# Kernel optimization log

Measured on AMD Instinct MI355X. Metric: run time of the kernel, lower is better.

## Reference

```python
import jax, jax.numpy as jnp
import numpy as np
import math

B, H, W, D = 4, 64, 64, 256
N, K, V = 8, 32, 32


def setup_inputs() -> dict:
    key = jax.random.key(0)
    ks = jax.random.split(key, 7)
    blob = jax.random.normal(ks[0], (B, H, W, D), dtype=jnp.float32)
    # 1x1 conv kernels == dense [D, out] matrices; glorot-ish scale
    s = 1.0 / math.sqrt(D)
    wq = jax.random.normal(ks[1], (D, N * K), dtype=jnp.float32) * s
    wk = jax.random.normal(ks[2], (D, N * K), dtype=jnp.float32) * s
    wv = jax.random.normal(ks[3], (D, N * V), dtype=jnp.float32) * s
    bq = jnp.zeros((N * K,), jnp.float32)
    bk = jnp.zeros((N * K,), jnp.float32)
    bv = jnp.zeros((N * V,), jnp.float32)
    return {"blob": blob, "wq": wq, "bq": bq, "wk": wk, "bk": bk, "wv": wv, "bv": bv}


def _maxpool2x2(x):
    # MaxPool2D with pool_size=strides=(2,2), VALID padding, NHWC
    return jax.lax.reduce_window(
        x, -jnp.inf, jax.lax.max,
        window_dimensions=(1, 2, 2, 1), window_strides=(1, 2, 2, 1), padding="VALID")


def reference(blob, wq, bq, wk, bk, wv, bv):
    H2, W2 = H // 2, W // 2
    # pooled query path
    q = _maxpool2x2(blob)                                   # [B,H2,W2,D]
    q = (q @ wq + bq).reshape(B, H2, W2, N, K)              # [B,H2,W2,N,K]
    q = q * (1.0 / math.sqrt(float(K)))
    # key/value paths (1x1 conv == per-pixel matmul); swish on value
    k = (blob @ wk + bk).reshape(B, H * W, N, K)            # [B,HW,N,K]
    v = jax.nn.swish(blob @ wv + bv).reshape(B, H * W, N, V)  # [B,HW,N,V]
    # cross-attention: contract K, outer product of pooled grid with full grid
    scores = jnp.einsum("bhwnk,bink->bhwin", q, k)          # [B,H2,W2,HW,N]
    attn = jax.nn.softmax(scores, axis=3)                   # softmax over HW
    out = jnp.einsum("bhwin,binv->bhwnv", attn, v)          # [B,H2,W2,N,V]
    return out.reshape(B, H2, W2, N * V)
```

## Files before the change

kernel.cpp:

```cpp
#include <hip/hip_runtime.h>


typedef _Float16 f16x8 __attribute__((ext_vector_type(8)));
typedef _Float16 f16x4 __attribute__((ext_vector_type(4)));
typedef float    f32x4 __attribute__((ext_vector_type(4)));

#define F16(x) static_cast<_Float16>(x)

#if __has_builtin(__builtin_amdgcn_exp2f)
#define EXP2(x) __builtin_amdgcn_exp2f(x)
#else
#define EXP2(x) exp2f(x)
#endif

__device__ __forceinline__ void gl_lds16(const void* g, void* l) {
    __builtin_amdgcn_global_load_lds(
        (const __attribute__((address_space(1))) unsigned int*)g,
        (__attribute__((address_space(3))) unsigned int*)l, 16, 0, 0);
}

__global__ __launch_bounds__(256) void prep_kernel(
    const float* __restrict__ wq, const float* __restrict__ wk,
    const float* __restrict__ wv, _Float16* __restrict__ wt) {
    __shared__ float t[32][33];
    const int blk = blockIdx.x;
    const int mat = blk >> 6;
    const int tile = blk & 63;
    const int d0 = (tile >> 3) * 32, o0 = (tile & 7) * 32;
    const float* w = (mat == 0) ? wq : (mat == 1 ? wk : wv);
    const int tx = threadIdx.x & 31, ty = threadIdx.x >> 5;
#pragma unroll
    for (int i = 0; i < 4; ++i)
        t[ty + i * 8][tx] = w[(d0 + ty + i * 8) * 256 + o0 + tx];
    __syncthreads();
#pragma unroll
    for (int i = 0; i < 4; ++i)
        wt[(mat << 16) + (o0 + ty + i * 8) * 256 + d0 + tx] = (_Float16)t[tx][ty + i * 8];
}

__global__ __launch_bounds__(256) void proj_kernel(
    const float* __restrict__ blob, const _Float16* __restrict__ wt,
    const float* __restrict__ bq, const float* __restrict__ bk, const float* __restrict__ bv,
    _Float16* __restrict__ qo, _Float16* __restrict__ ko, _Float16* __restrict__ vo) {
    const int lane = threadIdx.x & 63, wid = threadIdx.x >> 6;
    const int quad = lane >> 4, l16 = lane & 15;
    int jb = blockIdx.x;
    int job, rowblk;
    if (jb < 128)      { job = 0; rowblk = jb; }
    else if (jb < 640) { job = 1; rowblk = jb - 128; }
    else               { job = 2; rowblk = jb - 640; }
    const int rowbase = rowblk * 32;
    const int colbase = wid * 64;
    const _Float16* wmat = wt + ((size_t)job << 16);
    const float* bias = (job == 0) ? bq : (job == 1 ? bk : bv);

    f32x4 acc[2][4];
#pragma unroll
    for (int mc = 0; mc < 2; ++mc)
#pragma unroll
        for (int nt = 0; nt < 4; ++nt) acc[mc][nt] = (f32x4){0.f, 0.f, 0.f, 0.f};

    const float* a0[2];
#pragma unroll
    for (int mc = 0; mc < 2; ++mc) {
        const int m = rowbase + mc * 16 + l16;
        if (job == 0) {
            const int bb = m >> 10, y = (m >> 5) & 31, x = m & 31;
            a0[mc] = blob + (((bb * 64 + 2 * y) * 64) + 2 * x) * 256;
        } else {
            a0[mc] = blob + (size_t)m * 256;
        }
    }

#pragma unroll 2
    for (int kc = 0; kc < 8; ++kc) {
        f16x8 bf[4];
#pragma unroll
        for (int nt = 0; nt < 4; ++nt)
            bf[nt] = *(const f16x8*)(wmat + (colbase + nt * 16 + l16) * 256 + kc * 32 + quad * 8);
#pragma unroll
        for (int mc = 0; mc < 2; ++mc) {
            const float* ap = a0[mc] + kc * 32 + quad * 8;
            float va[8];
            if (job == 0) {
                float4 p0 = *(const float4*)(ap);
                float4 p1 = *(const float4*)(ap + 4);
                float4 q0 = *(const float4*)(ap + 256);
                float4 q1 = *(const float4*)(ap + 260);
                float4 r0 = *(const float4*)(ap + 16384);
                float4 r1 = *(const float4*)(ap + 16388);
                float4 s0 = *(const float4*)(ap + 16640);
                float4 s1 = *(const float4*)(ap + 16644);
                va[0] = fmaxf(fmaxf(p0.x, q0.x), fmaxf(r0.x, s0.x));
                va[1] = fmaxf(fmaxf(p0.y, q0.y), fmaxf(r0.y, s0.y));
                va[2] = fmaxf(fmaxf(p0.z, q0.z), fmaxf(r0.z, s0.z));
                va[3] = fmaxf(fmaxf(p0.w, q0.w), fmaxf(r0.w, s0.w));
                va[4] = fmaxf(fmaxf(p1.x, q1.x), fmaxf(r1.x, s1.x));
                va[5] = fmaxf(fmaxf(p1.y, q1.y), fmaxf(r1.y, s1.y));
                va[6] = fmaxf(fmaxf(p1.z, q1.z), fmaxf(r1.z, s1.z));
                va[7] = fmaxf(fmaxf(p1.w, q1.w), fmaxf(r1.w, s1.w));
            } else {
                float4 f0 = *(const float4*)(ap);
                float4 f1 = *(const float4*)(ap + 4);
                va[0] = f0.x; va[1] = f0.y; va[2] = f0.z; va[3] = f0.w;
                va[4] = f1.x; va[5] = f1.y; va[6] = f1.z; va[7] = f1.w;
            }
            auto c0 = __builtin_amdgcn_cvt_pkrtz(va[0], va[1]);
            auto c1 = __builtin_amdgcn_cvt_pkrtz(va[2], va[3]);
            auto c2 = __builtin_amdgcn_cvt_pkrtz(va[4], va[5]);
            auto c3 = __builtin_amdgcn_cvt_pkrtz(va[6], va[7]);
            f16x8 af = {F16(c0[0]), F16(c0[1]), F16(c1[0]), F16(c1[1]),
                        F16(c2[0]), F16(c2[1]), F16(c3[0]), F16(c3[1])};
#pragma unroll
            for (int nt = 0; nt < 4; ++nt)
                acc[mc][nt] = __builtin_amdgcn_mfma_f32_16x16x32_f16(af, bf[nt], acc[mc][nt], 0, 0, 0);
        }
    }

#pragma unroll
    for (int nt = 0; nt < 4; ++nt) {
        const int o = colbase + nt * 16 + l16;
        const float bs = bias[o];
        const int nh = o >> 5, kk = o & 31;
#pragma unroll
        for (int mc = 0; mc < 2; ++mc) {
            if (job == 0) {
#pragma unroll
                for (int r = 0; r < 4; ++r) {
                    const int grow = rowbase + mc * 16 + quad * 4 + r;
                    const float x = (acc[mc][nt][r] + bs) * 0.25503508f;
                    const int bb = grow >> 10, mm = grow & 1023;
                    qo[(((bb * 8 + nh) * 1024 + mm) << 5) + kk] = (_Float16)x;
                }
            } else if (job == 1) {
#pragma unroll
                for (int r = 0; r < 4; ++r) {
                    const int grow = rowbase + mc * 16 + quad * 4 + r;
                    const float x = acc[mc][nt][r] + bs;
                    const int bb = grow >> 12, ii = grow & 4095;
                    ko[(((bb * 8 + nh) * 4096 + ii) << 5) + kk] = (_Float16)x;
                }
            } else {
                const int grow0 = rowbase + mc * 16 + quad * 4;
                const int bb = grow0 >> 12, i0 = grow0 & 4095;
                f16x4 pv;
#pragma unroll
                for (int r = 0; r < 4; ++r) {
                    float x = acc[mc][nt][r] + bs;
                    const float sg = 1.0f / (1.0f + __expf(-x));
                    pv[r] = (_Float16)(x * sg);
                }
                *(f16x4*)(vo + (((size_t)(bb * 8 + nh) * 32 + kk) << 12) + i0) = pv;
            }
        }
    }
}

__global__ __launch_bounds__(512, 4) void attn_kernel(
    const _Float16* __restrict__ qb,
    const _Float16* __restrict__ kb,
    const _Float16* __restrict__ vt,
    float* __restrict__ out) {
    __shared__ __align__(16) char pool[49152];

    const int tid = threadIdx.x;
    const int lane = tid & 63, wid = tid >> 6;
    const int quad = lane >> 4, l16 = lane & 15;
    const int bn = blockIdx.x & 31, mt = blockIdx.x >> 5;
    const int b = bn >> 3, n = bn & 7;
    const int m0 = mt * 64;
    const int rg = wid & 3, kc = wid >> 2;

    const _Float16* gsrc[2];
    int ldsoff[2], adv[2];
#pragma unroll
    for (int jj = 0; jj < 2; ++jj) {
        const int j = wid + jj * 8;
        const int kcj = j >> 3, sub = j & 7;
        const int gl = (sub & 3) * 64 + lane;
        if (sub < 4) {
            const int k = gl >> 2, c = ((gl & 3) - (k >> 2)) & 3;
            gsrc[jj]   = kb + ((size_t)bn << 17) + (size_t)(kcj * 2048 + k) * 32 + c * 8;
            ldsoff[jj] = kcj * 24576 + gl * 16;
            adv[jj] = 2048;
        } else {
            const int v = gl >> 3, c = ((gl & 7) - v) & 7;
            gsrc[jj]   = vt + ((size_t)bn << 17) + (size_t)v * 4096 + kcj * 2048 + c * 8;
            ldsoff[jj] = kcj * 24576 + 4096 + gl * 16;
            adv[jj] = 64;
        }
    }

    const f16x8 qf = *(const f16x8*)(qb + (((size_t)(bn << 10) + m0 + rg * 16 + l16) << 5) + quad * 8);

    const int kread = kc * 24576 + l16 * 64 + ((quad + (l16 >> 2)) & 3) * 16;
    const int vread = kc * 24576 + 4096 + l16 * 128 + (quad & 1) * 8;
    const int r0 = (quad >> 1) + l16;

#pragma unroll
    for (int p = 0; p < 2; ++p)
#pragma unroll
        for (int jj = 0; jj < 2; ++jj) {
            gl_lds16(gsrc[jj], pool + ldsoff[jj] + p * 8192);
            gsrc[jj] += adv[jj];
        }
    asm volatile("s_waitcnt vmcnt(2)\n\ts_barrier" ::: "memory");

    f32x4 acc0 = (f32x4){0.f, 0.f, 0.f, 0.f};
    f32x4 acc1 = acc0;
    float ps0 = 0.f;

    for (int s = 0; s < 32; ++s) {
        if (s < 30) {
            const int nb = ((s + 2) % 3) * 8192;
#pragma unroll
            for (int jj = 0; jj < 2; ++jj) {
                gl_lds16(gsrc[jj], pool + ldsoff[jj] + nb);
                gsrc[jj] += adv[jj];
            }
        }
        const char* kbase = pool + kread + (s % 3) * 8192;
        const char* vbase = pool + vread + (s % 3) * 8192;
#pragma unroll
        for (int tloc = 0; tloc < 4; ++tloc) {
            const f16x8 kf = *(const f16x8*)(kbase + tloc * 1024);
            const int rot = ((2 * tloc + r0) & 7) * 16;
            const f16x4 va0 = *(const f16x4*)(vbase + rot);
            const f16x4 va1 = *(const f16x4*)(vbase + rot + 2048);

            f32x4 s0 = __builtin_amdgcn_mfma_f32_16x16x32_f16(kf, qf, (f32x4){0.f,0.f,0.f,0.f}, 0, 0, 0);
            const float p0 = EXP2(s0[0]), p1 = EXP2(s0[1]), p2 = EXP2(s0[2]), p3 = EXP2(s0[3]);
            ps0 += (p0 + p1) + (p2 + p3);
            auto e0 = __builtin_amdgcn_cvt_pkrtz(p0, p1);
            auto e1 = __builtin_amdgcn_cvt_pkrtz(p2, p3);
            const f16x4 pb = {F16(e0[0]), F16(e0[1]), F16(e1[0]), F16(e1[1])};
            acc0 = __builtin_amdgcn_mfma_f32_16x16x16f16(va0, pb, acc0, 0, 0, 0);
            acc1 = __builtin_amdgcn_mfma_f32_16x16x16f16(va1, pb, acc1, 0, 0, 0);
        }
        if (s < 30)       asm volatile("s_waitcnt vmcnt(2)\n\ts_barrier" ::: "memory");
        else if (s == 30) asm volatile("s_waitcnt vmcnt(0)\n\ts_barrier" ::: "memory");
        else              asm volatile("s_barrier" ::: "memory");
    }

    float* num = (float*)pool;
    float* den = (float*)(pool + 64 * 33 * 4);
    for (int i = tid; i < 64 * 33 + 64; i += 512) ((float*)pool)[i] = 0.f;
    __syncthreads();

    ps0 += __shfl_xor(ps0, 16); ps0 += __shfl_xor(ps0, 32);

    const int m = rg * 16 + l16;
#pragma unroll
    for (int r = 0; r < 4; ++r) {
        atomicAdd(&num[m * 33 + quad * 4 + r], acc0[r]);
        atomicAdd(&num[m * 33 + 16 + quad * 4 + r], acc1[r]);
    }
    if (quad == 0) atomicAdd(&den[m], ps0);
    __syncthreads();

    {
        const int mloc = tid >> 3, v4 = (tid & 7) * 4;
        const float inv = 1.0f / den[mloc];
        const float* nr = num + mloc * 33 + v4;
        float4 o = {nr[0] * inv, nr[1] * inv, nr[2] * inv, nr[3] * inv};
        *(float4*)(out + (((size_t)(b << 10) + m0 + mloc) << 8) + n * 32 + v4) = o;
    }
}

extern "C" void kernel_launch(void* const* d_in, const int* in_sizes, int n_in,
                              void* d_out, int out_size, void* d_ws, size_t ws_size,
                              hipStream_t stream) {
    const float* blob = (const float*)d_in[0];
    const float* wq = (const float*)d_in[1];
    const float* bq = (const float*)d_in[2];
    const float* wk = (const float*)d_in[3];
    const float* bk = (const float*)d_in[4];
    const float* wv = (const float*)d_in[5];
    const float* bv = (const float*)d_in[6];
    float* out = (float*)d_out;

    char* ws = (char*)d_ws;
    _Float16* wt = (_Float16*)(ws);
    _Float16* ko = (_Float16*)(ws + 393216);
    _Float16* vo = (_Float16*)(ws + 8781824);
    _Float16* qo = (_Float16*)(ws + 17170432);

    prep_kernel<<<192, 256, 0, stream>>>(wq, wk, wv, wt);
    proj_kernel<<<1152, 256, 0, stream>>>(blob, wt, bq, bk, bv, qo, ko, vo);
    attn_kernel<<<512, 512, 0, stream>>>(qo, ko, vo, out);
}
```

Baseline: 161.6 us.

## Stage A tile through LDS with double buffering and 64-row blocks in projection

The projection kernel now covers 64 rows per block instead of 32, halving the grid. Each thread loads one 8-element fp32 slice of the activation (max-pooled for the query job), converts it to fp16 and writes it into a swizzled, double-buffered LDS tile. All four waves then read it from LDS instead of each wave reloading the activations from global memory. Weight fragments and the next activation slice are prefetched one step ahead around a barrier. This cuts redundant global activation traffic and overlaps loads with MFMA work, at the cost of per-step barriers, more accumulator registers and fewer blocks for latency hiding.

```diff
diff --git a/kernel.cpp b/kernel.cpp
--- a/kernel.cpp
+++ b/kernel.cpp
@@ -42,79 +42,108 @@
     const float* __restrict__ blob, const _Float16* __restrict__ wt,
     const float* __restrict__ bq, const float* __restrict__ bk, const float* __restrict__ bv,
     _Float16* __restrict__ qo, _Float16* __restrict__ ko, _Float16* __restrict__ vo) {
-    const int lane = threadIdx.x & 63, wid = threadIdx.x >> 6;
+    __shared__ __align__(16) char atile[2][4096];
+
+    const int tid = threadIdx.x;
+    const int lane = tid & 63, wid = tid >> 6;
     const int quad = lane >> 4, l16 = lane & 15;
     int jb = blockIdx.x;
     int job, rowblk;
-    if (jb < 128)      { job = 0; rowblk = jb; }
-    else if (jb < 640) { job = 1; rowblk = jb - 128; }
-    else               { job = 2; rowblk = jb - 640; }
-    const int rowbase = rowblk * 32;
+    if (jb < 64)       { job = 0; rowblk = jb; }
+    else if (jb < 320) { job = 1; rowblk = jb - 64; }
+    else               { job = 2; rowblk = jb - 320; }
+    const int rowbase = rowblk * 64;
     const int colbase = wid * 64;
     const _Float16* wmat = wt + ((size_t)job << 16);
     const float* bias = (job == 0) ? bq : (job == 1 ? bk : bv);
 
-    f32x4 acc[2][4];
-#pragma unroll
-    for (int mc = 0; mc < 2; ++mc)
+    const int srow = tid >> 2, sc8 = tid & 3;
+    const int sslot = srow * 4 + ((sc8 + (srow >> 2)) & 3);
+    const float* aptr;
+    if (job == 0) {
+        const int grow = rowbase + srow;
+        const int bb = grow >> 10, y = (grow >> 5) & 31, x = grow & 31;
+        aptr = blob + (((bb * 64 + 2 * y) * 64) + 2 * x) * 256 + sc8 * 8;
+    } else {
+        aptr = blob + (size_t)(rowbase + srow) * 256 + sc8 * 8;
+    }
+
+    const _Float16* wptr[4];
+#pragma unroll
+    for (int nt = 0; nt < 4; ++nt)
+        wptr[nt] = wmat + (size_t)(colbase + nt * 16 + l16) * 256 + quad * 8;
+
+    const int aread = l16 * 64 + ((quad + (l16 >> 2)) & 3) * 16;
+
+    f32x4 acc[4][4];
+#pragma unroll
+    for (int mc = 0; mc < 4; ++mc)
 #pragma unroll
         for (int nt = 0; nt < 4; ++nt) acc[mc][nt] = (f32x4){0.f, 0.f, 0.f, 0.f};
 
-    const float* a0[2];
-#pragma unroll
-    for (int mc = 0; mc < 2; ++mc) {
-        const int m = rowbase + mc * 16 + l16;
+    f16x8 wf[2][4];
+    float4 ar[2][2];
+
+    auto A_LOAD = [&](int t, float4* dst) {
+        const float* p = aptr + t * 32;
         if (job == 0) {
-            const int bb = m >> 10, y = (m >> 5) & 31, x = m & 31;
-            a0[mc] = blob + (((bb * 64 + 2 * y) * 64) + 2 * x) * 256;
+            float4 a0 = *(const float4*)(p);
+            float4 a1 = *(const float4*)(p + 4);
+            float4 b0 = *(const float4*)(p + 256);
+            float4 b1 = *(const float4*)(p + 260);
+            float4 c0 = *(const float4*)(p + 16384);
+            float4 c1 = *(const float4*)(p + 16388);
+            float4 d0 = *(const float4*)(p + 16640);
+            float4 d1 = *(const float4*)(p + 16644);
+            dst[0].x = fmaxf(fmaxf(a0.x, b0.x), fmaxf(c0.x, d0.x));
+            dst[0].y = fmaxf(fmaxf(a0.y, b0.y), fmaxf(c0.y, d0.y));
+            dst[0].z = fmaxf(fmaxf(a0.z, b0.z), fmaxf(c0.z, d0.z));
+            dst[0].w = fmaxf(fmaxf(a0.w, b0.w), fmaxf(c0.w, d0.w));
+            dst[1].x = fmaxf(fmaxf(a1.x, b1.x), fmaxf(c1.x, d1.x));
+            dst[1].y = fmaxf(fmaxf(a1.y, b1.y), fmaxf(c1.y, d1.y));
+            dst[1].z = fmaxf(fmaxf(a1.z, b1.z), fmaxf(c1.z, d1.z));
+            dst[1].w = fmaxf(fmaxf(a1.w, b1.w), fmaxf(c1.w, d1.w));
         } else {
-            a0[mc] = blob + (size_t)m * 256;
-        }
-    }
-
-#pragma unroll 2
-    for (int kc = 0; kc < 8; ++kc) {
-        f16x8 bf[4];
-#pragma unroll
-        for (int nt = 0; nt < 4; ++nt)
-            bf[nt] = *(const f16x8*)(wmat + (colbase + nt * 16 + l16) * 256 + kc * 32 + quad * 8);
-#pragma unroll
-        for (int mc = 0; mc < 2; ++mc) {
-            const float* ap = a0[mc] + kc * 32 + quad * 8;
-            float va[8];
-            if (job == 0) {
-                float4 p0 = *(const float4*)(ap);
-                float4 p1 = *(const float4*)(ap + 4);
-                float4 q0 = *(const float4*)(ap + 256);
-                float4 q1 = *(const float4*)(ap + 260);
-                float4 r0 = *(const float4*)(ap + 16384);
-                float4 r1 = *(const float4*)(ap + 16388);
-                float4 s0 = *(const float4*)(ap + 16640);
-                float4 s1 = *(const float4*)(ap + 16644);
-                va[0] = fmaxf(fmaxf(p0.x, q0.x), fmaxf(r0.x, s0.x));
-                va[1] = fmaxf(fmaxf(p0.y, q0.y), fmaxf(r0.y, s0.y));
-                va[2] = fmaxf(fmaxf(p0.z, q0.z), fmaxf(r0.z, s0.z));
-                va[3] = fmaxf(fmaxf(p0.w, q0.w), fmaxf(r0.w, s0.w));
-                va[4] = fmaxf(fmaxf(p1.x, q1.x), fmaxf(r1.x, s1.x));
-                va[5] = fmaxf(fmaxf(p1.y, q1.y), fmaxf(r1.y, s1.y));
-                va[6] = fmaxf(fmaxf(p1.z, q1.z), fmaxf(r1.z, s1.z));
-                va[7] = fmaxf(fmaxf(p1.w, q1.w), fmaxf(r1.w, s1.w));
-            } else {
-                float4 f0 = *(const float4*)(ap);
-                float4 f1 = *(const float4*)(ap + 4);
-                va[0] = f0.x; va[1] = f0.y; va[2] = f0.z; va[3] = f0.w;
-                va[4] = f1.x; va[5] = f1.y; va[6] = f1.z; va[7] = f1.w;
-            }
-            auto c0 = __builtin_amdgcn_cvt_pkrtz(va[0], va[1]);
-            auto c1 = __builtin_amdgcn_cvt_pkrtz(va[2], va[3]);
-            auto c2 = __builtin_amdgcn_cvt_pkrtz(va[4], va[5]);
-            auto c3 = __builtin_amdgcn_cvt_pkrtz(va[6], va[7]);
-            f16x8 af = {F16(c0[0]), F16(c0[1]), F16(c1[0]), F16(c1[1]),
-                        F16(c2[0]), F16(c2[1]), F16(c3[0]), F16(c3[1])};
+            dst[0] = *(const float4*)(p);
+            dst[1] = *(const float4*)(p + 4);
+        }
+    };
+    auto A_WRITE = [&](int buf, const float4* src) {
+        auto c0 = __builtin_amdgcn_cvt_pkrtz(src[0].x, src[0].y);
+        auto c1 = __builtin_amdgcn_cvt_pkrtz(src[0].z, src[0].w);
+        auto c2 = __builtin_amdgcn_cvt_pkrtz(src[1].x, src[1].y);
+        auto c3 = __builtin_amdgcn_cvt_pkrtz(src[1].z, src[1].w);
+        f16x8 v = {F16(c0[0]), F16(c0[1]), F16(c1[0]), F16(c1[1]),
+                   F16(c2[0]), F16(c2[1]), F16(c3[0]), F16(c3[1])};
+        *(f16x8*)(atile[buf] + sslot * 16) = v;
+    };
+    auto W_LOAD = [&](int t, f16x8* dst) {
+#pragma unroll
+        for (int nt = 0; nt < 4; ++nt) dst[nt] = *(const f16x8*)(wptr[nt] + t * 32);
+    };
+
+    W_LOAD(0, wf[0]);
+    A_LOAD(0, ar[0]);
+    A_WRITE(0, ar[0]);
+    A_LOAD(1, ar[1]);
+    asm volatile("s_waitcnt lgkmcnt(0)\n\ts_barrier" ::: "memory");
+
+#pragma unroll
+    for (int s = 0; s < 8; ++s) {
+        if (s < 7) W_LOAD(s + 1, wf[(s + 1) & 1]);
+        f16x8 af[4];
+#pragma unroll
+        for (int mc = 0; mc < 4; ++mc)
+            af[mc] = *(const f16x8*)(atile[s & 1] + mc * 1024 + aread);
+#pragma unroll
+        for (int mc = 0; mc < 4; ++mc)
 #pragma unroll
             for (int nt = 0; nt < 4; ++nt)
-                acc[mc][nt] = __builtin_amdgcn_mfma_f32_16x16x32_f16(af, bf[nt], acc[mc][nt], 0, 0, 0);
-        }
+                acc[mc][nt] = __builtin_amdgcn_mfma_f32_16x16x32_f16(
+                    af[mc], wf[s & 1][nt], acc[mc][nt], 0, 0, 0);
+        if (s < 7) A_WRITE((s + 1) & 1, ar[(s + 1) & 1]);
+        if (s < 6) A_LOAD(s + 2, ar[s & 1]);
+        if (s < 7) asm volatile("s_waitcnt lgkmcnt(0)\n\ts_barrier" ::: "memory");
     }
 
 #pragma unroll
@@ -123,7 +152,7 @@
         const float bs = bias[o];
         const int nh = o >> 5, kk = o & 31;
 #pragma unroll
-        for (int mc = 0; mc < 2; ++mc) {
+        for (int mc = 0; mc < 4; ++mc) {
             if (job == 0) {
 #pragma unroll
                 for (int r = 0; r < 4; ++r) {
@@ -286,6 +315,6 @@
     _Float16* qo = (_Float16*)(ws + 17170432);
 
     prep_kernel<<<192, 256, 0, stream>>>(wq, wk, wv, wt);
-    proj_kernel<<<1152, 256, 0, stream>>>(blob, wt, bq, bk, bv, qo, ko, vo);
+    proj_kernel<<<576, 256, 0, stream>>>(blob, wt, bq, bk, bv, qo, ko, vo);
     attn_kernel<<<512, 512, 0, stream>>>(qo, ko, vo, out);
 }
```

Result: faster. 137.2 us (-15.1%).
